# Optimization experiments

Measured on AMD Instinct MI355X. Metric: run time of the kernel, lower is better.

## Reference

```python
import jax, jax.numpy as jnp
import numpy as np

B, T, E = 16, 2048, 768   # batch, frames, encoder dim
C, D = 504, 256           # num_classes, final_dim
EPS = 1e-8                # torch cosine_similarity eps
LOGIT_TEMP = 0.1


def _normalize(v):
    n = jnp.maximum(jnp.linalg.norm(v, axis=-1, keepdims=True), EPS)
    return v / n


def _compute_logits(proj_x, target, emb):
    # proj_x: [N, D], target: [N] int, emb: [C, D]
    pxn = _normalize(proj_x)
    embn = _normalize(emb)
    pos = jnp.take(embn, target, axis=0)            # [N, D]
    pos_logit = jnp.sum(pxn * pos, axis=-1)          # [N]
    neg_logits = pxn @ embn.T                        # [N, C] fused normalize+matmul
    # neg_is_pos: class row identical to the positive row (distinct random rows => class == label)
    neg_is_pos = jnp.arange(emb.shape[0])[None, :] == target[:, None]
    neg_logits = jnp.where(neg_is_pos, -jnp.inf, neg_logits)
    logits = jnp.concatenate([pos_logit[:, None], neg_logits], axis=1)  # [N, 1+C]
    return logits / LOGIT_TEMP


def setup_inputs() -> dict:
    key = jax.random.key(0)
    k1, k2, k3, k4, k5 = jax.random.split(key, 5)
    x = jax.random.normal(k1, (B, T, E), dtype=jnp.float32)
    label = jax.random.randint(k2, (B, T), 0, C)
    mask_m = jnp.ones((B, T), dtype=bool)
    mask_u = jnp.ones((B, T), dtype=bool)
    bound = 1.0 / np.sqrt(E)
    W = jax.random.uniform(k3, (D, E), minval=-bound, maxval=bound, dtype=jnp.float32)
    b = jax.random.uniform(k4, (D,), minval=-bound, maxval=bound, dtype=jnp.float32)
    emb = jax.random.uniform(k5, (C, D), dtype=jnp.float32)  # torch.nn.init.uniform_ default [0,1)
    return {"x": x, "label": label, "mask_m": mask_m, "mask_u": mask_u,
            "W": W, "b": b, "emb": emb}


def reference(x, label, mask_m, mask_u, W, b, emb):
    proj_x = jnp.einsum('bte,de->btd', x, W) + b        # final_proj
    pf = proj_x.reshape(-1, D)
    lf = label.reshape(-1)
    idx_m = jnp.nonzero(mask_m.reshape(-1))[0]          # concrete masks -> static shapes
    idx_u = jnp.nonzero(mask_u.reshape(-1))[0]
    logit_m = _compute_logits(pf[idx_m], lf[idx_m], emb)
    logit_u = _compute_logits(pf[idx_u], lf[idx_u], emb)
    return (logit_m, logit_u)
```

## Files before the change

### kernel.cpp

```cpp
#include <hip/hip_runtime.h>
#include <hip/hip_bf16.h>
#include <math.h>

#define N_ROWS 32768
#define E_DIM  768
#define D_DIM  256
#define C_CLS  504
#define C_PAD  512
#define N_OUT  505
#define EPS    1e-8f
#define NEG_BIG (-1e30f)

typedef __attribute__((ext_vector_type(8))) __bf16 bf16x8;
typedef __attribute__((ext_vector_type(4))) float f32x4;

__global__ __launch_bounds__(256) void convert_w_kernel(const float* __restrict__ W,
                                                        __bf16* __restrict__ Wh) {
    const int idx = blockIdx.x * 256 + threadIdx.x;
    const float4 v = ((const float4*)W)[idx];
    union { __bf16 h[4]; uint2 u; } pk;
    pk.h[0] = (__bf16)v.x; pk.h[1] = (__bf16)v.y;
    pk.h[2] = (__bf16)v.z; pk.h[3] = (__bf16)v.w;
    ((uint2*)Wh)[idx] = pk.u;
}

__global__ __launch_bounds__(64) void embnorm_kernel(const float* __restrict__ emb,
                                                     __bf16* __restrict__ embnh) {
    const int c = blockIdx.x;
    const int lane = threadIdx.x;
    union { __bf16 h[4]; uint2 u; } pk;
    if (c < C_CLS) {
        const float4 v = ((const float4*)(emb + (size_t)c * D_DIM))[lane];
        float s = v.x * v.x + v.y * v.y + v.z * v.z + v.w * v.w;
        #pragma unroll
        for (int off = 32; off; off >>= 1) s += __shfl_xor(s, off);
        const float inv = 1.0f / fmaxf(sqrtf(s), EPS);
        pk.h[0] = (__bf16)(v.x * inv); pk.h[1] = (__bf16)(v.y * inv);
        pk.h[2] = (__bf16)(v.z * inv); pk.h[3] = (__bf16)(v.w * inv);
    } else {
        pk.h[0] = (__bf16)0.0f; pk.h[1] = (__bf16)0.0f;
        pk.h[2] = (__bf16)0.0f; pk.h[3] = (__bf16)0.0f;
    }
    ((uint2*)(embnh + (size_t)c * D_DIM))[lane] = pk.u;
}

__global__ __launch_bounds__(256) void gemm1_mfma(const float* __restrict__ x,
                                                  const __bf16* __restrict__ Wh,
                                                  const float* __restrict__ bias,
                                                  __bf16* __restrict__ projn) {
    __shared__ float sos[4][32];

    const int tid  = threadIdx.x;
    const int w    = tid >> 6;
    const int lane = tid & 63;
    const int l15  = lane & 15;
    const int quad = lane >> 4;
    const int row0 = blockIdx.x * 32;
    const int c0   = w * 64;

    const float* ap0 = x + (size_t)(row0 + l15) * E_DIM + quad * 8;
    const float* ap1 = ap0 + 16 * E_DIM;
    const __bf16* bp[4];
    #pragma unroll
    for (int n = 0; n < 4; ++n)
        bp[n] = Wh + (size_t)(c0 + n * 16 + l15) * E_DIM + quad * 8;

    f32x4 acc[2][4] = {};

    #pragma unroll
    for (int k0 = 0; k0 < E_DIM; k0 += 32) {
        const float4 u0 = *(const float4*)(ap0 + k0);
        const float4 u1 = *(const float4*)(ap0 + k0 + 4);
        const float4 u2 = *(const float4*)(ap1 + k0);
        const float4 u3 = *(const float4*)(ap1 + k0 + 4);
        bf16x8 bfv[4];
        #pragma unroll
        for (int n = 0; n < 4; ++n) bfv[n] = *(const bf16x8*)(bp[n] + k0);

        union { __bf16 h[8]; bf16x8 v; } a0, a1;
        a0.h[0] = (__bf16)u0.x; a0.h[1] = (__bf16)u0.y; a0.h[2] = (__bf16)u0.z; a0.h[3] = (__bf16)u0.w;
        a0.h[4] = (__bf16)u1.x; a0.h[5] = (__bf16)u1.y; a0.h[6] = (__bf16)u1.z; a0.h[7] = (__bf16)u1.w;
        a1.h[0] = (__bf16)u2.x; a1.h[1] = (__bf16)u2.y; a1.h[2] = (__bf16)u2.z; a1.h[3] = (__bf16)u2.w;
        a1.h[4] = (__bf16)u3.x; a1.h[5] = (__bf16)u3.y; a1.h[6] = (__bf16)u3.z; a1.h[7] = (__bf16)u3.w;

        #pragma unroll
        for (int n = 0; n < 4; ++n)
            acc[0][n] = __builtin_amdgcn_mfma_f32_16x16x32_bf16(a0.v, bfv[n], acc[0][n], 0, 0, 0);
        #pragma unroll
        for (int n = 0; n < 4; ++n)
            acc[1][n] = __builtin_amdgcn_mfma_f32_16x16x32_bf16(a1.v, bfv[n], acc[1][n], 0, 0, 0);
    }

    float bv[4];
    #pragma unroll
    for (int n = 0; n < 4; ++n) bv[n] = bias[c0 + n * 16 + l15];

    float ss[2][4];
    #pragma unroll
    for (int m = 0; m < 2; ++m)
        #pragma unroll
        for (int r = 0; r < 4; ++r) {
            float t = 0.0f;
            #pragma unroll
            for (int n = 0; n < 4; ++n) {
                const float v = acc[m][n][r] + bv[n];
                acc[m][n][r] = v;
                t += v * v;
            }
            t += __shfl_xor(t, 1);
            t += __shfl_xor(t, 2);
            t += __shfl_xor(t, 4);
            t += __shfl_xor(t, 8);
            ss[m][r] = t;
        }
    if (l15 == 0) {
        #pragma unroll
        for (int m = 0; m < 2; ++m)
            #pragma unroll
            for (int r = 0; r < 4; ++r)
                sos[w][m * 16 + quad * 4 + r] = ss[m][r];
    }
    __syncthreads();
    #pragma unroll
    for (int m = 0; m < 2; ++m)
        #pragma unroll
        for (int r = 0; r < 4; ++r) {
            const int R = m * 16 + quad * 4 + r;
            const float tot = sos[0][R] + sos[1][R] + sos[2][R] + sos[3][R];
            const float inv = 1.0f / fmaxf(sqrtf(tot), EPS);
            __bf16* op = projn + (size_t)(row0 + R) * D_DIM + c0 + l15;
            #pragma unroll
            for (int n = 0; n < 4; ++n)
                op[n * 16] = (__bf16)(acc[m][n][r] * inv);
        }
}

__global__ __launch_bounds__(256) void gemm2_mfma(const __bf16* __restrict__ projn,
                                                  const __bf16* __restrict__ embnh,
                                                  const int* __restrict__ label,
                                                  float* __restrict__ outm,
                                                  float* __restrict__ outu) {
    __shared__ int lab_s[32];

    const int tid  = threadIdx.x;
    const int w    = tid >> 6;
    const int lane = tid & 63;
    const int l15  = lane & 15;
    const int quad = lane >> 4;
    const int row0 = blockIdx.x * 32;
    const int c0   = w * 128;

    if (tid < 32) lab_s[tid] = label[row0 + tid];

    const __bf16* ap0 = projn + (size_t)(row0 + l15) * D_DIM + quad * 8;
    const __bf16* ap1 = ap0 + 16 * D_DIM;
    const __bf16* bp[8];
    #pragma unroll
    for (int n = 0; n < 8; ++n)
        bp[n] = embnh + (size_t)(c0 + n * 16 + l15) * D_DIM + quad * 8;

    f32x4 acc[2][8] = {};
    __syncthreads();

    #pragma unroll
    for (int k0 = 0; k0 < D_DIM; k0 += 32) {
        const bf16x8 a0 = *(const bf16x8*)(ap0 + k0);
        const bf16x8 a1 = *(const bf16x8*)(ap1 + k0);
        bf16x8 bfv[8];
        #pragma unroll
        for (int n = 0; n < 8; ++n) bfv[n] = *(const bf16x8*)(bp[n] + k0);
        #pragma unroll
        for (int n = 0; n < 8; ++n) {
            acc[0][n] = __builtin_amdgcn_mfma_f32_16x16x32_bf16(a0, bfv[n], acc[0][n], 0, 0, 0);
            acc[1][n] = __builtin_amdgcn_mfma_f32_16x16x32_bf16(a1, bfv[n], acc[1][n], 0, 0, 0);
        }
    }

    #pragma unroll
    for (int m = 0; m < 2; ++m)
        #pragma unroll
        for (int r = 0; r < 4; ++r) {
            const int Rl  = m * 16 + quad * 4 + r;
            const int lab = lab_s[Rl];
            const size_t base = (size_t)(row0 + Rl) * N_OUT;
            #pragma unroll
            for (int n = 0; n < 8; ++n) {
                const int c = c0 + n * 16 + l15;
                if (c < C_CLS) {
                    const float val = acc[m][n][r] * 10.0f;
                    const bool pos = (c == lab);
                    const float neg = pos ? NEG_BIG : val;
                    outm[base + 1 + c] = neg;
                    outu[base + 1 + c] = neg;
                    if (pos) { outm[base] = val; outu[base] = val; }
                }
            }
        }
}

extern "C" void kernel_launch(void* const* d_in, const int* in_sizes, int n_in,
                              void* d_out, int out_size, void* d_ws, size_t ws_size,
                              hipStream_t stream) {
    const float* x     = (const float*)d_in[0];
    const int*   label = (const int*)d_in[1];
    const float* W     = (const float*)d_in[4];
    const float* b     = (const float*)d_in[5];
    const float* emb   = (const float*)d_in[6];
    float* out = (float*)d_out;

    char* ws = (char*)d_ws;
    __bf16* Wh    = (__bf16*)ws;
    __bf16* embnh = (__bf16*)(ws + 393216);
    __bf16* projn = (__bf16*)(ws + 393216 + 262144);

    convert_w_kernel<<<192, 256, 0, stream>>>(W, Wh);
    embnorm_kernel<<<C_PAD, 64, 0, stream>>>(emb, embnh);
    gemm1_mfma<<<N_ROWS / 32, 256, 0, stream>>>(x, Wh, b, projn);
    gemm2_mfma<<<N_ROWS / 32, 256, 0, stream>>>(
        projn, embnh, label, out, out + (size_t)N_ROWS * N_OUT);
}
```

Before: 337.4 us.

## Stage GEMM tiles in LDS via direct global-to-LDS loads and coalesce output stores

Adds a separate pass that converts x to bf16, then rewrites both GEMMs to stage 64-row A tiles and full B tiles into swizzled shared memory using global_load_lds, with 64-row blocks. The second GEMM is split across a 2D grid over class halves and writes its logits through an LDS buffer so the stores along each output row are coalesced. The goal is better operand reuse and fewer uncoalesced writes. The cost is an extra full read and write of x in the conversion pass and more synchronisation per block.

```diff
diff --git a/kernel.cpp b/kernel.cpp
--- a/kernel.cpp
+++ b/kernel.cpp
@@ -14,6 +14,13 @@
 typedef __attribute__((ext_vector_type(8))) __bf16 bf16x8;
 typedef __attribute__((ext_vector_type(4))) float f32x4;
 
+#define MFMA16(a, b, c) __builtin_amdgcn_mfma_f32_16x16x32_bf16((a), (b), (c), 0, 0, 0)
+
+#define GLDS16(g, l)                                                   \
+    __builtin_amdgcn_global_load_lds(                                  \
+        (const __attribute__((address_space(1))) void*)(g),            \
+        (__attribute__((address_space(3))) void*)(l), 16, 0, 0)
+
 __global__ __launch_bounds__(256) void convert_w_kernel(const float* __restrict__ W,
                                                         __bf16* __restrict__ Wh) {
     const int idx = blockIdx.x * 256 + threadIdx.x;
@@ -24,6 +31,19 @@
     ((uint2*)Wh)[idx] = pk.u;
 }
 
+__global__ __launch_bounds__(256) void convert_x_kernel(const float* __restrict__ x,
+                                                        __bf16* __restrict__ xh) {
+    const int idx = blockIdx.x * 256 + threadIdx.x;
+    const float4 v0 = ((const float4*)x)[idx * 2];
+    const float4 v1 = ((const float4*)x)[idx * 2 + 1];
+    union { __bf16 h[8]; uint4 u; } pk;
+    pk.h[0] = (__bf16)v0.x; pk.h[1] = (__bf16)v0.y;
+    pk.h[2] = (__bf16)v0.z; pk.h[3] = (__bf16)v0.w;
+    pk.h[4] = (__bf16)v1.x; pk.h[5] = (__bf16)v1.y;
+    pk.h[6] = (__bf16)v1.z; pk.h[7] = (__bf16)v1.w;
+    ((uint4*)xh)[idx] = pk.u;
+}
+
 __global__ __launch_bounds__(64) void embnorm_kernel(const float* __restrict__ emb,
                                                      __bf16* __restrict__ embnh) {
     const int c = blockIdx.x;
@@ -44,60 +64,70 @@
     ((uint2*)(embnh + (size_t)c * D_DIM))[lane] = pk.u;
 }
 
-__global__ __launch_bounds__(256) void gemm1_mfma(const float* __restrict__ x,
+
+__global__ __launch_bounds__(256) void gemm1_mfma(const __bf16* __restrict__ xh,
                                                   const __bf16* __restrict__ Wh,
                                                   const float* __restrict__ bias,
                                                   __bf16* __restrict__ projn) {
-    __shared__ float sos[4][32];
+    __shared__ __bf16 As[64 * 64];
+    __shared__ __bf16 Bs[256 * 64];
+    __shared__ float sos[4][64];
 
     const int tid  = threadIdx.x;
     const int w    = tid >> 6;
     const int lane = tid & 63;
     const int l15  = lane & 15;
     const int quad = lane >> 4;
-    const int row0 = blockIdx.x * 32;
-    const int c0   = w * 64;
-
-    const float* ap0 = x + (size_t)(row0 + l15) * E_DIM + quad * 8;
-    const float* ap1 = ap0 + 16 * E_DIM;
-    const __bf16* bp[4];
-    #pragma unroll
-    for (int n = 0; n < 4; ++n)
-        bp[n] = Wh + (size_t)(c0 + n * 16 + l15) * E_DIM + quad * 8;
-
-    f32x4 acc[2][4] = {};
-
-    #pragma unroll
-    for (int k0 = 0; k0 < E_DIM; k0 += 32) {
-        const float4 u0 = *(const float4*)(ap0 + k0);
-        const float4 u1 = *(const float4*)(ap0 + k0 + 4);
-        const float4 u2 = *(const float4*)(ap1 + k0);
-        const float4 u3 = *(const float4*)(ap1 + k0 + 4);
-        bf16x8 bfv[4];
-        #pragma unroll
-        for (int n = 0; n < 4; ++n) bfv[n] = *(const bf16x8*)(bp[n] + k0);
-
-        union { __bf16 h[8]; bf16x8 v; } a0, a1;
-        a0.h[0] = (__bf16)u0.x; a0.h[1] = (__bf16)u0.y; a0.h[2] = (__bf16)u0.z; a0.h[3] = (__bf16)u0.w;
-        a0.h[4] = (__bf16)u1.x; a0.h[5] = (__bf16)u1.y; a0.h[6] = (__bf16)u1.z; a0.h[7] = (__bf16)u1.w;
-        a1.h[0] = (__bf16)u2.x; a1.h[1] = (__bf16)u2.y; a1.h[2] = (__bf16)u2.z; a1.h[3] = (__bf16)u2.w;
-        a1.h[4] = (__bf16)u3.x; a1.h[5] = (__bf16)u3.y; a1.h[6] = (__bf16)u3.z; a1.h[7] = (__bf16)u3.w;
-
-        #pragma unroll
-        for (int n = 0; n < 4; ++n)
-            acc[0][n] = __builtin_amdgcn_mfma_f32_16x16x32_bf16(a0.v, bfv[n], acc[0][n], 0, 0, 0);
-        #pragma unroll
-        for (int n = 0; n < 4; ++n)
-            acc[1][n] = __builtin_amdgcn_mfma_f32_16x16x32_bf16(a1.v, bfv[n], acc[1][n], 0, 0, 0);
+    const int row0 = blockIdx.x * 64;
+
+    f32x4 acc[4][4] = {};
+
+    for (int k0 = 0; k0 < E_DIM; k0 += 64) {
+        #pragma unroll
+        for (int c = 0; c < 2; ++c) {
+            const int o   = tid * 16 + c * 4096;
+            const int row = o >> 7;
+            const int sc  = ((o >> 4) & 7) ^ (row & 7);
+            GLDS16(xh + (size_t)(row0 + row) * E_DIM + k0 + sc * 8,
+                   (char*)As + c * 4096 + (w << 10));
+        }
+        #pragma unroll
+        for (int c = 0; c < 8; ++c) {
+            const int o   = tid * 16 + c * 4096;
+            const int row = o >> 7;
+            const int sc  = ((o >> 4) & 7) ^ (row & 7);
+            GLDS16(Wh + (size_t)row * E_DIM + k0 + sc * 8,
+                   (char*)Bs + c * 4096 + (w << 10));
+        }
+        __syncthreads();
+
+        #pragma unroll
+        for (int kk = 0; kk < 2; ++kk) {
+            const int chunk = (quad + 4 * kk) ^ (l15 & 7);
+            bf16x8 af[4], bf[4];
+            #pragma unroll
+            for (int m = 0; m < 4; ++m)
+                af[m] = *(const bf16x8*)((const char*)As +
+                          (m * 16 + l15) * 128 + (chunk << 4));
+            #pragma unroll
+            for (int n = 0; n < 4; ++n)
+                bf[n] = *(const bf16x8*)((const char*)Bs +
+                          (w * 64 + n * 16 + l15) * 128 + (chunk << 4));
+            #pragma unroll
+            for (int m = 0; m < 4; ++m)
+                #pragma unroll
+                for (int n = 0; n < 4; ++n)
+                    acc[m][n] = MFMA16(af[m], bf[n], acc[m][n]);
+        }
+        __syncthreads();
     }
 
     float bv[4];
     #pragma unroll
-    for (int n = 0; n < 4; ++n) bv[n] = bias[c0 + n * 16 + l15];
-
-    float ss[2][4];
-    #pragma unroll
-    for (int m = 0; m < 2; ++m)
+    for (int n = 0; n < 4; ++n) bv[n] = bias[w * 64 + n * 16 + l15];
+
+    #pragma unroll
+    for (int m = 0; m < 4; ++m)
         #pragma unroll
         for (int r = 0; r < 4; ++r) {
             float t = 0.0f;
@@ -111,24 +141,17 @@
             t += __shfl_xor(t, 2);
             t += __shfl_xor(t, 4);
             t += __shfl_xor(t, 8);
-            ss[m][r] = t;
-        }
-    if (l15 == 0) {
-        #pragma unroll
-        for (int m = 0; m < 2; ++m)
-            #pragma unroll
-            for (int r = 0; r < 4; ++r)
-                sos[w][m * 16 + quad * 4 + r] = ss[m][r];
-    }
+            if (l15 == 0) sos[w][m * 16 + quad * 4 + r] = t;
+        }
     __syncthreads();
     #pragma unroll
-    for (int m = 0; m < 2; ++m)
+    for (int m = 0; m < 4; ++m)
         #pragma unroll
         for (int r = 0; r < 4; ++r) {
             const int R = m * 16 + quad * 4 + r;
             const float tot = sos[0][R] + sos[1][R] + sos[2][R] + sos[3][R];
             const float inv = 1.0f / fmaxf(sqrtf(tot), EPS);
-            __bf16* op = projn + (size_t)(row0 + R) * D_DIM + c0 + l15;
+            __bf16* op = projn + (size_t)(row0 + R) * D_DIM + w * 64 + l15;
             #pragma unroll
             for (int n = 0; n < 4; ++n)
                 op[n * 16] = (__bf16)(acc[m][n][r] * inv);
@@ -140,62 +163,110 @@
                                                   const int* __restrict__ label,
                                                   float* __restrict__ outm,
                                                   float* __restrict__ outu) {
-    __shared__ int lab_s[32];
+    __shared__ char smem[40960];
+    __shared__ int labs[64];
+    __bf16* As = (__bf16*)smem;
+    __bf16* Bs = (__bf16*)(smem + 8192);
+    float (*obuf)[260] = (float (*)[260])smem;
+    float* posv = (float*)(smem + 33280);
 
     const int tid  = threadIdx.x;
     const int w    = tid >> 6;
     const int lane = tid & 63;
     const int l15  = lane & 15;
     const int quad = lane >> 4;
-    const int row0 = blockIdx.x * 32;
-    const int c0   = w * 128;
-
-    if (tid < 32) lab_s[tid] = label[row0 + tid];
-
-    const __bf16* ap0 = projn + (size_t)(row0 + l15) * D_DIM + quad * 8;
-    const __bf16* ap1 = ap0 + 16 * D_DIM;
-    const __bf16* bp[8];
-    #pragma unroll
-    for (int n = 0; n < 8; ++n)
-        bp[n] = embnh + (size_t)(c0 + n * 16 + l15) * D_DIM + quad * 8;
-
-    f32x4 acc[2][8] = {};
-    __syncthreads();
-
-    #pragma unroll
-    for (int k0 = 0; k0 < D_DIM; k0 += 32) {
-        const bf16x8 a0 = *(const bf16x8*)(ap0 + k0);
-        const bf16x8 a1 = *(const bf16x8*)(ap1 + k0);
-        bf16x8 bfv[8];
-        #pragma unroll
-        for (int n = 0; n < 8; ++n) bfv[n] = *(const bf16x8*)(bp[n] + k0);
-        #pragma unroll
-        for (int n = 0; n < 8; ++n) {
-            acc[0][n] = __builtin_amdgcn_mfma_f32_16x16x32_bf16(a0, bfv[n], acc[0][n], 0, 0, 0);
-            acc[1][n] = __builtin_amdgcn_mfma_f32_16x16x32_bf16(a1, bfv[n], acc[1][n], 0, 0, 0);
-        }
-    }
-
-    #pragma unroll
-    for (int m = 0; m < 2; ++m)
-        #pragma unroll
-        for (int r = 0; r < 4; ++r) {
-            const int Rl  = m * 16 + quad * 4 + r;
-            const int lab = lab_s[Rl];
-            const size_t base = (size_t)(row0 + Rl) * N_OUT;
-            #pragma unroll
-            for (int n = 0; n < 8; ++n) {
-                const int c = c0 + n * 16 + l15;
-                if (c < C_CLS) {
+    const int row0 = blockIdx.x * 64;
+    const int c0   = blockIdx.y * 256;
+
+    if (tid < 64) labs[tid] = label[row0 + tid];
+
+    f32x4 acc[4][4] = {};
+
+    for (int k0 = 0; k0 < D_DIM; k0 += 64) {
+        #pragma unroll
+        for (int c = 0; c < 2; ++c) {
+            const int o   = tid * 16 + c * 4096;
+            const int row = o >> 7;
+            const int sc  = ((o >> 4) & 7) ^ (row & 7);
+            GLDS16(projn + (size_t)(row0 + row) * D_DIM + k0 + sc * 8,
+                   (char*)As + c * 4096 + (w << 10));
+        }
+        #pragma unroll
+        for (int c = 0; c < 8; ++c) {
+            const int o   = tid * 16 + c * 4096;
+            const int row = o >> 7;
+            const int sc  = ((o >> 4) & 7) ^ (row & 7);
+            GLDS16(embnh + (size_t)(c0 + row) * D_DIM + k0 + sc * 8,
+                   (char*)Bs + c * 4096 + (w << 10));
+        }
+        __syncthreads();
+
+        #pragma unroll
+        for (int kk = 0; kk < 2; ++kk) {
+            const int chunk = (quad + 4 * kk) ^ (l15 & 7);
+            bf16x8 af[4], bf[4];
+            #pragma unroll
+            for (int m = 0; m < 4; ++m)
+                af[m] = *(const bf16x8*)((const char*)As +
+                          (m * 16 + l15) * 128 + (chunk << 4));
+            #pragma unroll
+            for (int n = 0; n < 4; ++n)
+                bf[n] = *(const bf16x8*)((const char*)Bs +
+                          (w * 64 + n * 16 + l15) * 128 + (chunk << 4));
+            #pragma unroll
+            for (int m = 0; m < 4; ++m)
+                #pragma unroll
+                for (int n = 0; n < 4; ++n)
+                    acc[m][n] = MFMA16(af[m], bf[n], acc[m][n]);
+        }
+        __syncthreads();
+    }
+
+    #pragma unroll
+    for (int g = 0; g < 2; ++g) {
+        #pragma unroll
+        for (int mi = 0; mi < 2; ++mi) {
+            const int m = g * 2 + mi;
+            #pragma unroll
+            for (int r = 0; r < 4; ++r) {
+                const int lrow = mi * 16 + quad * 4 + r;
+                const int lab  = labs[g * 32 + lrow];
+                #pragma unroll
+                for (int n = 0; n < 4; ++n) {
+                    const int cl = w * 64 + n * 16 + l15;
+                    const int c  = c0 + cl;
                     const float val = acc[m][n][r] * 10.0f;
                     const bool pos = (c == lab);
-                    const float neg = pos ? NEG_BIG : val;
-                    outm[base + 1 + c] = neg;
-                    outu[base + 1 + c] = neg;
-                    if (pos) { outm[base] = val; outu[base] = val; }
+                    obuf[lrow][cl] = pos ? NEG_BIG : val;
+                    if (pos) posv[lrow] = val;
                 }
             }
         }
+        __syncthreads();
+        {
+            const int c = c0 + tid;
+            if (c < C_CLS) {
+                #pragma unroll
+                for (int r = 0; r < 32; ++r) {
+                    const size_t base = (size_t)(row0 + g * 32 + r) * N_OUT;
+                    const float v = obuf[r][tid];
+                    outm[base + 1 + c] = v;
+                    outu[base + 1 + c] = v;
+                }
+            }
+        }
+        if (tid < 32) {
+            const int gr = g * 32 + tid;
+            const int lab = labs[gr];
+            if (lab >= c0 && lab < c0 + 256) {
+                const size_t base = (size_t)(row0 + gr) * N_OUT;
+                const float v = posv[tid];
+                outm[base] = v;
+                outu[base] = v;
+            }
+        }
+        __syncthreads();
+    }
 }
 
 extern "C" void kernel_launch(void* const* d_in, const int* in_sizes, int n_in,
@@ -212,10 +283,12 @@
     __bf16* Wh    = (__bf16*)ws;
     __bf16* embnh = (__bf16*)(ws + 393216);
     __bf16* projn = (__bf16*)(ws + 393216 + 262144);
+    __bf16* xh    = (__bf16*)(ws + 393216 + 262144 + 16777216);
 
     convert_w_kernel<<<192, 256, 0, stream>>>(W, Wh);
     embnorm_kernel<<<C_PAD, 64, 0, stream>>>(emb, embnh);
-    gemm1_mfma<<<N_ROWS / 32, 256, 0, stream>>>(x, Wh, b, projn);
-    gemm2_mfma<<<N_ROWS / 32, 256, 0, stream>>>(
+    convert_x_kernel<<<12288, 256, 0, stream>>>(x, xh);
+    gemm1_mfma<<<N_ROWS / 64, 256, 0, stream>>>(xh, Wh, b, projn);
+    gemm2_mfma<<<dim3(N_ROWS / 64, 2), 256, 0, stream>>>(
         projn, embnh, label, out, out + (size_t)N_ROWS * N_OUT);
 }
```

Result: faster. 286.0 us (-15.2%).
